# Kernel tuning notes

Measured on AMD Instinct MI355X. Metric: run time of the kernel, lower is better.

## Reference

```python
import jax, jax.numpy as jnp
import numpy as np

B, S, D, C = 16, 1024, 768, 2


def setup_inputs() -> dict:
    key = jax.random.key(0)
    ks = jax.random.split(key, 6)
    sc = 1.0 / np.sqrt(D)
    return {
        "tokens": jax.random.normal(ks[0], (B, S, D), jnp.float32),
        "Wk": jax.random.normal(ks[1], (D, D), jnp.float32) * sc,
        "bk": jnp.zeros((D,), jnp.float32),
        "Wq": jax.random.normal(ks[2], (D, D), jnp.float32) * sc,
        "bq": jnp.zeros((D,), jnp.float32),
        "Wv": jax.random.normal(ks[3], (D, D), jnp.float32) * sc,
        "bv": jnp.zeros((D,), jnp.float32),
        "ln_g": jnp.ones((S, D), jnp.float32),
        "ln_b": jnp.zeros((S, D), jnp.float32),
        "W_sgsa": jax.random.normal(ks[4], (D, 1), jnp.float32) * sc,
        "b_sgsa": jnp.zeros((1,), jnp.float32),
        "W_fnn": jax.random.normal(ks[5], (4 * D, C), jnp.float32) * (1.0 / np.sqrt(4 * D)),
        "b_fnn": jnp.zeros((C,), jnp.float32),
    }


def reference(tokens, Wk, bk, Wq, bq, Wv, bv, ln_g, ln_b, W_sgsa, b_sgsa, W_fnn, b_fnn):
    fact = 1.0 / jnp.sqrt(jnp.asarray(D, tokens.dtype))
    # --- token-wise single-head attention ---
    K = tokens @ Wk + bk                                  # [B,S,D]
    Q = tokens @ Wq + bq
    V = tokens @ Wv + bv
    att = jax.nn.softmax(jnp.einsum('bsd,btd->bst', Q, K) * fact, axis=-1)  # [B,S,S]
    out = jnp.einsum('bst,btd->bsd', att, V)              # [B,S,D]
    # --- LayerNorm over last two dims (S,D) jointly, eps=1e-8 ---
    mu = jnp.mean(out, axis=(1, 2), keepdims=True)
    var = jnp.var(out, axis=(1, 2), keepdims=True)
    out_ln = (out - mu) / jnp.sqrt(var + 1e-8) * ln_g + ln_b
    # --- feature-wise attention (same K/Q/V weights, transposed bmm) ---
    K_N = out_ln @ Wk + bk
    Q_N = out_ln @ Wq + bq
    V_N = out_ln @ Wv + bv
    att_N = jax.nn.softmax(jnp.einsum('bsd,bse->bde', Q_N, K_N) * fact, axis=-1)  # [B,D,D]
    out_N = jnp.einsum('bsd,bde->bse', V_N, att_N)        # [B,S,D]
    # --- SGSA gating ---
    gate = out_N @ W_sgsa + b_sgsa                        # [B,S,1]
    out_sgsa = gate * out_N                               # [B,S,D]
    # --- concat, dual pooling, FC ---
    cat = jnp.concatenate([tokens, out_sgsa], axis=2)     # [B,S,2D]
    pooled = jnp.concatenate([jnp.mean(cat, axis=1), jnp.max(cat, axis=1)], axis=1)  # [B,4D]
    return pooled @ W_fnn + b_fnn                         # [B,C]
```

## Files before the change

### kernel.cpp

```cpp
#include <hip/hip_runtime.h>

#define BB 16
#define SS 1024
#define DD 768

typedef _Float16 f16x4 __attribute__((ext_vector_type(4)));
typedef _Float16 f16x8 __attribute__((ext_vector_type(8)));
typedef float f32x4 __attribute__((ext_vector_type(4)));

__device__ __forceinline__ void gload_lds16(const void* g, void* l) {
  __builtin_amdgcn_global_load_lds(
      (const __attribute__((address_space(1))) unsigned int*)g,
      (__attribute__((address_space(3))) unsigned int*)l, 16, 0, 0);
}

template<int OUTM, int BIAS>
__global__ __launch_bounds__(512) void gemm256(
    const _Float16* __restrict__ A, long long aB,
    const _Float16* __restrict__ Bt, long long bB,
    const float* __restrict__ bias, int biasB,
    void* __restrict__ Cv, long long cB,
    int M, int N, int K)
{
  __shared__ __attribute__((aligned(16))) _Float16 lds[65536];
  const int t = threadIdx.x;
  int z, m0, n0;
  if (OUTM == 3 || OUTM == 4) {
    const int lin = blockIdx.x + 9 * blockIdx.y;
    const int xcd = lin & 7, idx = lin >> 3;
    const int mt  = xcd * 8 + idx / 9;
    const int zn  = idx % 9;
    z  = zn / 3;
    n0 = (zn % 3) * 256;
    m0 = mt * 256;
  } else {
    z = blockIdx.z;
    m0 = blockIdx.x * 256;
    n0 = blockIdx.y * 256;
  }
  const _Float16* Ab = A + (size_t)z * aB;
  const _Float16* Bb = Bt + (size_t)z * bB;

  const int l = t & 63, w = t >> 6;
  const int wr = (w >> 2) * 128, wc = (w & 3) * 64;
  const int lrow = l & 15, kq = l >> 4;
  const int p2 = lrow >> 1;
  const int qread = ((lrow & 1) << 2) | (kq ^ (p2 & 3));
  const int fragoff = p2 * 128 + qread * 16;

  const int sp = t >> 3, sq = t & 7;
  const int srow = 2 * sp + (sq >> 2);
  const int schk = (sq & 3) ^ (sp & 3);
  const size_t ldK = (size_t)K * 2;
  const char* pA0 = (const char*)Ab + (size_t)(m0 + srow) * ldK + schk * 16;
  const char* pA1 = pA0 + (size_t)128 * ldK;
  const char* pB0 = (const char*)Bb + (size_t)(n0 + srow) * ldK + schk * 16;
  const char* pB1 = pB0 + (size_t)128 * ldK;
  char* const ldsb = (char*)lds;
  const int dstt = t * 16;

  auto stg = [&](int mat, int s, int T, int sd) {
    const char* g0 = (mat ? pB0 : pA0) + (size_t)T * 128 + s * 64;
    const char* g1 = (mat ? pB1 : pA1) + (size_t)T * 128 + s * 64;
    char* d = ldsb + sd * 65536 + mat * 32768 + s * 16384 + dstt;
    gload_lds16(g0, d);
    gload_lds16(g1, d + 8192);
  };

  f32x4 acc[8][4] = {};
  f16x8 b0[4], b1[4], a00[4], a01[4], a10[4], a11[4];

  stg(0, 0, 0, 0); stg(1, 0, 0, 0); stg(0, 1, 0, 0); stg(1, 1, 0, 0);

  const int NT = K >> 6;
  for (int T = 0; T < NT; ++T) {
    const int sd = T & 1, sn = sd ^ 1;
    const char* Abase = ldsb + sd * 65536;
    const char* Bbase = Abase + 32768;
    const bool pf = (T + 1) < NT;

    asm volatile("s_waitcnt vmcnt(0)" ::: "memory");
    __builtin_amdgcn_s_barrier();
    asm volatile("" ::: "memory");
    if (pf) {
      stg(0, 0, T + 1, sn); stg(1, 0, T + 1, sn);
      stg(0, 1, T + 1, sn); stg(1, 1, T + 1, sn);
    }

    #pragma unroll
    for (int n = 0; n < 4; n++)
      b0[n]  = *(const f16x8*)(Bbase + (wc + n * 16) * 64 + fragoff);
    #pragma unroll
    for (int mi = 0; mi < 4; mi++)
      a00[mi] = *(const f16x8*)(Abase + (wr + mi * 16) * 64 + fragoff);
    #pragma unroll
    for (int mi = 0; mi < 4; mi++)
      a01[mi] = *(const f16x8*)(Abase + (wr + 64 + mi * 16) * 64 + fragoff);
    #pragma unroll
    for (int n = 0; n < 4; n++)
      b1[n]  = *(const f16x8*)(Bbase + 16384 + (wc + n * 16) * 64 + fragoff);
    #pragma unroll
    for (int mi = 0; mi < 4; mi++)
      a10[mi] = *(const f16x8*)(Abase + 16384 + (wr + mi * 16) * 64 + fragoff);
    #pragma unroll
    for (int mi = 0; mi < 4; mi++)
      a11[mi] = *(const f16x8*)(Abase + 16384 + (wr + 64 + mi * 16) * 64 + fragoff);

    __builtin_amdgcn_s_setprio(1);
    #pragma unroll
    for (int mi = 0; mi < 4; mi++)
      #pragma unroll
      for (int n = 0; n < 4; n++)
        acc[mi][n] = __builtin_amdgcn_mfma_f32_16x16x32_f16(a00[mi], b0[n], acc[mi][n], 0, 0, 0);
    #pragma unroll
    for (int mi = 0; mi < 4; mi++)
      #pragma unroll
      for (int n = 0; n < 4; n++)
        acc[4 + mi][n] = __builtin_amdgcn_mfma_f32_16x16x32_f16(a01[mi], b0[n], acc[4 + mi][n], 0, 0, 0);
    #pragma unroll
    for (int mi = 0; mi < 4; mi++)
      #pragma unroll
      for (int n = 0; n < 4; n++)
        acc[mi][n] = __builtin_amdgcn_mfma_f32_16x16x32_f16(a10[mi], b1[n], acc[mi][n], 0, 0, 0);
    #pragma unroll
    for (int mi = 0; mi < 4; mi++)
      #pragma unroll
      for (int n = 0; n < 4; n++)
        acc[4 + mi][n] = __builtin_amdgcn_mfma_f32_16x16x32_f16(a11[mi], b1[n], acc[4 + mi][n], 0, 0, 0);
    __builtin_amdgcn_s_setprio(0);
  }

  const int crow = (l >> 4) * 4, ccol = l & 15;
  #pragma unroll
  for (int m = 0; m < 8; ++m) {
    const int rq = m0 + wr + (m >> 2) * 64 + (m & 3) * 16 + crow;
    #pragma unroll
    for (int n = 0; n < 4; ++n) {
      const int c = n0 + wc + n * 16 + ccol;
      const float bv = BIAS ? bias[(size_t)z * biasB + c] : 0.0f;
      if (OUTM == 0) {
        float* C = (float*)Cv + (size_t)z * cB;
        #pragma unroll
        for (int j = 0; j < 4; j++)
          C[(size_t)(rq + j) * N + c] = acc[m][n][j] + bv;
      } else {
        _Float16* C = (_Float16*)Cv + (size_t)z * cB;
        const bool tr = (OUTM == 3) ? (z == 2) : (z < 2);
        if (tr) {
          const int bq = rq >> 10, s = rq & 1023;
          f16x4 o;
          #pragma unroll
          for (int j = 0; j < 4; j++) o[j] = (_Float16)(acc[m][n][j] + bv);
          *(f16x4*)&C[((size_t)(bq * N + c) << 10) + s] = o;
        } else {
          #pragma unroll
          for (int j = 0; j < 4; j++)
            C[(size_t)(rq + j) * N + c] = (_Float16)(acc[m][n][j] + bv);
        }
      }
    }
  }
}

__global__ __launch_bounds__(256) void cast_f2h(const float* __restrict__ in,
                                                _Float16* __restrict__ outp, long long n4)
{
  for (long long i = (long long)blockIdx.x * 256 + threadIdx.x; i < n4;
       i += (long long)gridDim.x * 256) {
    float4 v = ((const float4*)in)[i];
    f16x4 r;
    r[0] = (_Float16)v.x; r[1] = (_Float16)v.y; r[2] = (_Float16)v.z; r[3] = (_Float16)v.w;
    ((f16x4*)outp)[i] = r;
  }
}

__global__ __launch_bounds__(256) void transpose_f2h(const float* __restrict__ in,
                                                     _Float16* __restrict__ outp, int R, int C)
{
  __shared__ float tile[32][33];
  const int r0 = blockIdx.y * 32, c0 = blockIdx.x * 32;
  const int tx = threadIdx.x & 31, ty = threadIdx.x >> 5;
  #pragma unroll
  for (int i = 0; i < 4; i++)
    tile[ty + i * 8][tx] = in[(size_t)(r0 + ty + i * 8) * C + c0 + tx];
  __syncthreads();
  #pragma unroll
  for (int i = 0; i < 4; i++)
    outp[(size_t)(c0 + ty + i * 8) * R + r0 + tx] = (_Float16)tile[tx][ty + i * 8];
}

__global__ __launch_bounds__(256) void transpose_b2h(const _Float16* __restrict__ in, long long inB,
                                                     _Float16* __restrict__ outp, long long outB,
                                                     int R, int C)
{
  __shared__ _Float16 tile[32][33];
  const _Float16* ib = in + (size_t)blockIdx.z * inB;
  _Float16* ob = outp + (size_t)blockIdx.z * outB;
  const int r0 = blockIdx.y * 32, c0 = blockIdx.x * 32;
  const int tx = threadIdx.x & 31, ty = threadIdx.x >> 5;
  #pragma unroll
  for (int i = 0; i < 4; i++)
    tile[ty + i * 8][tx] = ib[(size_t)(r0 + ty + i * 8) * C + c0 + tx];
  __syncthreads();
  #pragma unroll
  for (int i = 0; i < 4; i++)
    ob[(size_t)(c0 + ty + i * 8) * R + r0 + tx] = tile[tx][ty + i * 8];
}

__global__ void pack_bias(const float* __restrict__ a, const float* __restrict__ b,
                          const float* __restrict__ c, float* __restrict__ o)
{
  int t = blockIdx.x * 256 + threadIdx.x;
  if (t < 768) o[t] = a[t];
  else if (t < 1536) o[t] = b[t - 768];
  else if (t < 2304) o[t] = c[t - 1536];
}

template<int VPT>
__global__ __launch_bounds__(256) void softmax_f2h(const float* __restrict__ X,
                                                   _Float16* __restrict__ Y,
                                                   int L, float scale)
{
  const size_t base = (size_t)blockIdx.x * L;
  const int t = threadIdx.x;
  float v[VPT];
  float m = -3.4e38f;
  #pragma unroll
  for (int j = 0; j < VPT; j++) { v[j] = X[base + t + j * 256]; m = fmaxf(m, v[j]); }
  __shared__ float red[256];
  red[t] = m; __syncthreads();
  #pragma unroll
  for (int off = 128; off > 0; off >>= 1) {
    if (t < off) red[t] = fmaxf(red[t], red[t + off]);
    __syncthreads();
  }
  m = red[0]; __syncthreads();
  float s = 0.0f;
  #pragma unroll
  for (int j = 0; j < VPT; j++) { v[j] = __expf((v[j] - m) * scale); s += v[j]; }
  red[t] = s; __syncthreads();
  #pragma unroll
  for (int off = 128; off > 0; off >>= 1) {
    if (t < off) red[t] += red[t + off];
    __syncthreads();
  }
  const float inv = 1.0f / red[0];
  #pragma unroll
  for (int j = 0; j < VPT; j++) Y[base + t + j * 256] = (_Float16)(v[j] * inv);
}

__global__ __launch_bounds__(256) void ln_partial(const float* __restrict__ src,
                                                  float* __restrict__ part)
{
  const int b = blockIdx.y, ch = blockIdx.x;
  const float4* p = (const float4*)(src + (size_t)b * SS * DD) + (size_t)ch * 3072;
  const int t = threadIdx.x;
  float s = 0.0f, q = 0.0f;
  #pragma unroll
  for (int i = 0; i < 12; i++) {
    float4 v = p[t + i * 256];
    s += v.x + v.y + v.z + v.w;
    q += v.x * v.x + v.y * v.y + v.z * v.z + v.w * v.w;
  }
  __shared__ float rs[256], rq[256];
  rs[t] = s; rq[t] = q; __syncthreads();
  #pragma unroll
  for (int off = 128; off > 0; off >>= 1) {
    if (t < off) { rs[t] += rs[t + off]; rq[t] += rq[t + off]; }
    __syncthreads();
  }
  if (t == 0) { part[(b * 64 + ch) * 2] = rs[0]; part[(b * 64 + ch) * 2 + 1] = rq[0]; }
}

__global__ void ln_final(const float* __restrict__ part, float* __restrict__ stats)
{
  const int b = blockIdx.x, t = threadIdx.x;
  float s = part[(b * 64 + t) * 2];
  float q = part[(b * 64 + t) * 2 + 1];
  #pragma unroll
  for (int off = 32; off > 0; off >>= 1) { s += __shfl_down(s, off); q += __shfl_down(q, off); }
  if (t == 0) {
    const float invN = 1.0f / (float)(SS * DD);
    float mu = s * invN;
    float var = q * invN - mu * mu;
    stats[b * 2] = mu;
    stats[b * 2 + 1] = rsqrtf(var + 1e-8f);
  }
}

__global__ __launch_bounds__(256) void ln_apply_h(const float* __restrict__ src,
                                                  const float* __restrict__ g,
                                                  const float* __restrict__ bta,
                                                  const float* __restrict__ stats,
                                                  _Float16* __restrict__ dst)
{
  const long long n4 = (long long)BB * SS * DD / 4;
  const int SD4 = SS * DD / 4;
  for (long long i = (long long)blockIdx.x * 256 + threadIdx.x; i < n4;
       i += (long long)gridDim.x * 256) {
    const int b = (int)(i / SD4);
    const int sd4 = (int)(i - (long long)b * SD4);
    const float mu = stats[b * 2], rs = stats[b * 2 + 1];
    float4 v = ((const float4*)src)[i];
    float4 gg = ((const float4*)g)[sd4];
    float4 bb = ((const float4*)bta)[sd4];
    f16x4 r;
    r[0] = (_Float16)((v.x - mu) * rs * gg.x + bb.x);
    r[1] = (_Float16)((v.y - mu) * rs * gg.y + bb.y);
    r[2] = (_Float16)((v.z - mu) * rs * gg.z + bb.z);
    r[3] = (_Float16)((v.w - mu) * rs * gg.w + bb.w);
    ((f16x4*)dst)[i] = r;
  }
}

__global__ __launch_bounds__(256) void gate_k(const float* __restrict__ outN,
                                              const float* __restrict__ wsg,
                                              const float* __restrict__ bsg,
                                              float* __restrict__ gate)
{
  const int row = blockIdx.x * 4 + (threadIdx.x >> 6);
  const int l = threadIdx.x & 63;
  const float* src = outN + (size_t)row * DD;
  float s = 0.0f;
  #pragma unroll
  for (int i = 0; i < 12; i++) s += src[l + i * 64] * wsg[l + i * 64];
  #pragma unroll
  for (int off = 32; off > 0; off >>= 1) s += __shfl_down(s, off);
  if (l == 0) gate[row] = s + bsg[0];
}

__global__ __launch_bounds__(256) void pool_partial(const float* __restrict__ tokens,
                                                    const float* __restrict__ outN,
                                                    const float* __restrict__ gate,
                                                    float* __restrict__ part)
{
  const int b = blockIdx.y, ch = blockIdx.x, t = threadIdx.x;
  float st0 = 0, st1 = 0, st2 = 0, so0 = 0, so1 = 0, so2 = 0;
  float xt0 = -3.4e38f, xt1 = -3.4e38f, xt2 = -3.4e38f;
  float xo0 = -3.4e38f, xo1 = -3.4e38f, xo2 = -3.4e38f;
  const size_t rowbase = ((size_t)b * SS + ch * 32) * DD;
  for (int i = 0; i < 32; i++) {
    const float* tr = tokens + rowbase + (size_t)i * DD;
    const float* orw = outN + rowbase + (size_t)i * DD;
    const float g = gate[b * SS + ch * 32 + i];
    float t0 = tr[t], t1 = tr[t + 256], t2 = tr[t + 512];
    float o0 = orw[t] * g, o1 = orw[t + 256] * g, o2 = orw[t + 512] * g;
    st0 += t0; st1 += t1; st2 += t2;
    so0 += o0; so1 += o1; so2 += o2;
    xt0 = fmaxf(xt0, t0); xt1 = fmaxf(xt1, t1); xt2 = fmaxf(xt2, t2);
    xo0 = fmaxf(xo0, o0); xo1 = fmaxf(xo1, o1); xo2 = fmaxf(xo2, o2);
  }
  float* pb = part + (size_t)(b * 32 + ch) * 3072;
  pb[t] = st0;          pb[t + 256] = st1;          pb[t + 512] = st2;
  pb[768 + t] = so0;    pb[768 + t + 256] = so1;    pb[768 + t + 512] = so2;
  pb[1536 + t] = xt0;   pb[1536 + t + 256] = xt1;   pb[1536 + t + 512] = xt2;
  pb[2304 + t] = xo0;   pb[2304 + t + 256] = xo1;   pb[2304 + t + 512] = xo2;
}

__global__ __launch_bounds__(256) void pool_final(const float* __restrict__ part,
                                                  float* __restrict__ pooled)
{
  const int idx = blockIdx.x * 256 + threadIdx.x;
  const int b = idx / DD, d = idx - b * DD;
  float st = 0, so = 0, xt = -3.4e38f, xo = -3.4e38f;
  for (int ch = 0; ch < 32; ch++) {
    const float* pb = part + (size_t)(b * 32 + ch) * 3072;
    st += pb[d]; so += pb[768 + d];
    xt = fmaxf(xt, pb[1536 + d]); xo = fmaxf(xo, pb[2304 + d]);
  }
  const float inv = 1.0f / (float)SS;
  pooled[(size_t)b * 3072 + d]        = st * inv;
  pooled[(size_t)b * 3072 + 768 + d]  = so * inv;
  pooled[(size_t)b * 3072 + 1536 + d] = xt;
  pooled[(size_t)b * 3072 + 2304 + d] = xo;
}

__global__ __launch_bounds__(256) void fc_k(const float* __restrict__ pooled,
                                            const float* __restrict__ Wf,
                                            const float* __restrict__ bf,
                                            float* __restrict__ outp)
{
  const int b = blockIdx.x, t = threadIdx.x;
  float p0 = 0.0f, p1 = 0.0f;
  #pragma unroll
  for (int i = 0; i < 12; i++) {
    const int j = t + i * 256;
    const float pv = pooled[(size_t)b * 3072 + j];
    p0 += pv * Wf[j * 2];
    p1 += pv * Wf[j * 2 + 1];
  }
  __shared__ float r0[256], r1[256];
  r0[t] = p0; r1[t] = p1; __syncthreads();
  #pragma unroll
  for (int off = 128; off > 0; off >>= 1) {
    if (t < off) { r0[t] += r0[t + off]; r1[t] += r1[t + off]; }
    __syncthreads();
  }
  if (t == 0) {
    outp[b * 2 + 0] = r0[0] + bf[0];
    outp[b * 2 + 1] = r1[0] + bf[1];
  }
}

extern "C" void kernel_launch(void* const* d_in, const int* in_sizes, int n_in,
                              void* d_out, int out_size, void* d_ws, size_t ws_size,
                              hipStream_t stream)
{
  const float* tokens = (const float*)d_in[0];
  const float* Wk  = (const float*)d_in[1];
  const float* bk  = (const float*)d_in[2];
  const float* Wq  = (const float*)d_in[3];
  const float* bq  = (const float*)d_in[4];
  const float* Wv  = (const float*)d_in[5];
  const float* bv  = (const float*)d_in[6];
  const float* lng = (const float*)d_in[7];
  const float* lnb = (const float*)d_in[8];
  const float* Wsg = (const float*)d_in[9];
  const float* bsg = (const float*)d_in[10];
  const float* Wf  = (const float*)d_in[11];
  const float* bfn = (const float*)d_in[12];
  float* outp = (float*)d_out;
  (void)in_sizes; (void)n_in; (void)out_size; (void)ws_size;

  char* ws = (char*)d_ws;
  float*    R0   = (float*)(ws + 0);
  _Float16* R1   = (_Float16*)(ws + 67108864);
  _Float16* R2   = (_Float16*)(ws + 92274688);
  _Float16* R3   = (_Float16*)(ws + 117440512);
  _Float16* R4   = (_Float16*)(ws + 142606336);
  _Float16* R5   = (_Float16*)(ws + 167772160);
  _Float16* Wt   = (_Float16*)(ws + 201326592);
  float* bias3   = (float*)(ws + 204865536);
  float* part    = (float*)(ws + 204874752);
  float* stats   = (float*)(ws + 204882944);
  float* gate    = (float*)(ws + 204883072);
  float* ppart   = (float*)(ws + 204948608);
  float* pooled  = (float*)(ws + 211240064);

  const float fact = 0.036084391824351615f;
  const long long SD = (long long)SS * DD;
  const long long S2 = (long long)SS * SS;
  const long long D2 = (long long)DD * DD;
  const long long PL = (long long)BB * SD;

  cast_f2h<<<2048, 256, 0, stream>>>(tokens, R1, PL / 4);
  transpose_f2h<<<dim3(24, 24), 256, 0, stream>>>(Wk, Wt,               768, 768);
  transpose_f2h<<<dim3(24, 24), 256, 0, stream>>>(Wq, Wt + 589824,      768, 768);
  transpose_f2h<<<dim3(24, 24), 256, 0, stream>>>(Wv, Wt + 2 * 589824,  768, 768);
  pack_bias<<<9, 256, 0, stream>>>(bk, bq, bv, bias3);

  gemm256<3, 1><<<dim3(9, 64, 1), 512, 0, stream>>>(R1, 0, Wt, 589824, bias3, 768,
                                                    (void*)R2, PL, BB * SS, DD, DD);
  gemm256<0, 0><<<dim3(4, 4, 16), 512, 0, stream>>>(R3, SD, R2, SD, nullptr, 0,
                                                    (void*)R0, S2, SS, SS, DD);
  softmax_f2h<4><<<BB * SS, 256, 0, stream>>>(R0, R5, SS, fact);
  gemm256<0, 0><<<dim3(4, 3, 16), 512, 0, stream>>>(R5, S2, R4, SD, nullptr, 0,
                                                    (void*)R0, SD, SS, DD, SS);
  ln_partial<<<dim3(64, 16), 256, 0, stream>>>(R0, part);
  ln_final<<<16, 64, 0, stream>>>(part, stats);
  ln_apply_h<<<2048, 256, 0, stream>>>(R0, lng, lnb, stats, R1);

  gemm256<4, 1><<<dim3(9, 64, 1), 512, 0, stream>>>(R1, 0, Wt, 589824, bias3, 768,
                                                    (void*)R2, PL, BB * SS, DD, DD);
  gemm256<0, 0><<<dim3(3, 3, 16), 512, 0, stream>>>(R3, SD, R2, SD, nullptr, 0,
                                                    (void*)R0, D2, DD, DD, SS);
  softmax_f2h<3><<<BB * DD, 256, 0, stream>>>(R0, R5, DD, fact);
  transpose_b2h<<<dim3(24, 24, 16), 256, 0, stream>>>(R5, D2, R1, D2, DD, DD);
  gemm256<0, 0><<<dim3(4, 3, 16), 512, 0, stream>>>(R4, SD, R1, D2, nullptr, 0,
                                                    (void*)R0, SD, SS, DD, DD);

  gate_k<<<4096, 256, 0, stream>>>(R0, Wsg, bsg, gate);
  pool_partial<<<dim3(32, BB), 256, 0, stream>>>(tokens, R0, gate, ppart);
  pool_final<<<48, 256, 0, stream>>>(ppart, pooled);
  fc_k<<<16, 256, 0, stream>>>(pooled, Wf, bfn, outp);
}
```

Measured before the change: 440.0 us.

## Restructure GEMM main loop into four-phase ping-pong with staggered prefetch

Splits each K-tile iteration of the 256x256 GEMM into four MFMA quadrants, with barriers between them. Each quadrant's global-to-LDS prefetch is issued separately, two tiles ahead for some halves, using partial vmcnt waits instead of a full drain at the top of every iteration. The goal is to overlap LDS fragment reads and global loads with MFMA work and stop stalling on all outstanding loads each step. In exchange it adds many more block barriers per iteration and relies on subtle ordering of when buffers are reused, which risks races or barrier overhead.

```diff
diff --git a/kernel.cpp b/kernel.cpp
--- a/kernel.cpp
+++ b/kernel.cpp
@@ -44,9 +44,9 @@
   const int l = t & 63, w = t >> 6;
   const int wr = (w >> 2) * 128, wc = (w & 3) * 64;
   const int lrow = l & 15, kq = l >> 4;
-  const int p2 = lrow >> 1;
-  const int qread = ((lrow & 1) << 2) | (kq ^ (p2 & 3));
-  const int fragoff = p2 * 128 + qread * 16;
+  const int p2v = lrow >> 1;
+  const int qread = ((lrow & 1) << 2) | (kq ^ (p2v & 3));
+  const int fragoff = p2v * 128 + qread * 16;
 
   const int sp = t >> 3, sq = t & 7;
   const int srow = 2 * sp + (sq >> 2);
@@ -68,67 +68,118 @@
   };
 
   f32x4 acc[8][4] = {};
-  f16x8 b0[4], b1[4], a00[4], a01[4], a10[4], a11[4];
+  f16x8 a00[4], a01[4], a10[4], a11[4];
+  f16x8 b00[2], b01[2], b10[2], b11[2];
+
+#define MF(d, a, b) d = __builtin_amdgcn_mfma_f32_16x16x32_f16(a, b, d, 0, 0, 0)
 
   stg(0, 0, 0, 0); stg(1, 0, 0, 0); stg(0, 1, 0, 0); stg(1, 1, 0, 0);
+  stg(0, 0, 1, 1); stg(1, 0, 1, 1);
+  asm volatile("s_waitcnt vmcnt(4)" ::: "memory");
+  __builtin_amdgcn_s_barrier();
+  asm volatile("" ::: "memory");
 
   const int NT = K >> 6;
   for (int T = 0; T < NT; ++T) {
     const int sd = T & 1, sn = sd ^ 1;
     const char* Abase = ldsb + sd * 65536;
     const char* Bbase = Abase + 32768;
-    const bool pf = (T + 1) < NT;
-
-    asm volatile("s_waitcnt vmcnt(0)" ::: "memory");
+
+    #pragma unroll
+    for (int i = 0; i < 4; i++)
+      a00[i] = *(const f16x8*)(Abase + (wr + i * 16) * 64 + fragoff);
+    #pragma unroll
+    for (int i = 0; i < 4; i++)
+      a01[i] = *(const f16x8*)(Abase + 16384 + (wr + i * 16) * 64 + fragoff);
+    #pragma unroll
+    for (int n = 0; n < 2; n++)
+      b00[n] = *(const f16x8*)(Bbase + (wc + n * 16) * 64 + fragoff);
+    #pragma unroll
+    for (int n = 0; n < 2; n++)
+      b01[n] = *(const f16x8*)(Bbase + 16384 + (wc + n * 16) * 64 + fragoff);
+    if (T + 1 < NT) stg(0, 1, T + 1, sn);
+    __builtin_amdgcn_s_barrier();
+    asm volatile("s_waitcnt lgkmcnt(0)" ::: "memory");
+    __builtin_amdgcn_sched_barrier(0);
+    __builtin_amdgcn_s_setprio(1);
+    #pragma unroll
+    for (int i = 0; i < 4; i++) {
+      MF(acc[i][0], a00[i], b00[0]); MF(acc[i][1], a00[i], b00[1]);
+    }
+    #pragma unroll
+    for (int i = 0; i < 4; i++) {
+      MF(acc[i][0], a01[i], b01[0]); MF(acc[i][1], a01[i], b01[1]);
+    }
+    __builtin_amdgcn_s_setprio(0);
     __builtin_amdgcn_s_barrier();
     asm volatile("" ::: "memory");
-    if (pf) {
-      stg(0, 0, T + 1, sn); stg(1, 0, T + 1, sn);
-      stg(0, 1, T + 1, sn); stg(1, 1, T + 1, sn);
-    }
-
-    #pragma unroll
-    for (int n = 0; n < 4; n++)
-      b0[n]  = *(const f16x8*)(Bbase + (wc + n * 16) * 64 + fragoff);
-    #pragma unroll
-    for (int mi = 0; mi < 4; mi++)
-      a00[mi] = *(const f16x8*)(Abase + (wr + mi * 16) * 64 + fragoff);
-    #pragma unroll
-    for (int mi = 0; mi < 4; mi++)
-      a01[mi] = *(const f16x8*)(Abase + (wr + 64 + mi * 16) * 64 + fragoff);
-    #pragma unroll
-    for (int n = 0; n < 4; n++)
-      b1[n]  = *(const f16x8*)(Bbase + 16384 + (wc + n * 16) * 64 + fragoff);
-    #pragma unroll
-    for (int mi = 0; mi < 4; mi++)
-      a10[mi] = *(const f16x8*)(Abase + 16384 + (wr + mi * 16) * 64 + fragoff);
-    #pragma unroll
-    for (int mi = 0; mi < 4; mi++)
-      a11[mi] = *(const f16x8*)(Abase + 16384 + (wr + 64 + mi * 16) * 64 + fragoff);
-
+
+    #pragma unroll
+    for (int i = 0; i < 4; i++)
+      a10[i] = *(const f16x8*)(Abase + (wr + 64 + i * 16) * 64 + fragoff);
+    #pragma unroll
+    for (int i = 0; i < 4; i++)
+      a11[i] = *(const f16x8*)(Abase + 16384 + (wr + 64 + i * 16) * 64 + fragoff);
+    #pragma unroll
+    for (int n = 0; n < 2; n++)
+      b10[n] = *(const f16x8*)(Bbase + (wc + 32 + n * 16) * 64 + fragoff);
+    #pragma unroll
+    for (int n = 0; n < 2; n++)
+      b11[n] = *(const f16x8*)(Bbase + 16384 + (wc + 32 + n * 16) * 64 + fragoff);
+    if (T + 1 < NT) stg(1, 1, T + 1, sn);
+    __builtin_amdgcn_s_barrier();
+    asm volatile("s_waitcnt lgkmcnt(0)" ::: "memory");
+    __builtin_amdgcn_sched_barrier(0);
     __builtin_amdgcn_s_setprio(1);
     #pragma unroll
-    for (int mi = 0; mi < 4; mi++)
-      #pragma unroll
-      for (int n = 0; n < 4; n++)
-        acc[mi][n] = __builtin_amdgcn_mfma_f32_16x16x32_f16(a00[mi], b0[n], acc[mi][n], 0, 0, 0);
-    #pragma unroll
-    for (int mi = 0; mi < 4; mi++)
-      #pragma unroll
-      for (int n = 0; n < 4; n++)
-        acc[4 + mi][n] = __builtin_amdgcn_mfma_f32_16x16x32_f16(a01[mi], b0[n], acc[4 + mi][n], 0, 0, 0);
-    #pragma unroll
-    for (int mi = 0; mi < 4; mi++)
-      #pragma unroll
-      for (int n = 0; n < 4; n++)
-        acc[mi][n] = __builtin_amdgcn_mfma_f32_16x16x32_f16(a10[mi], b1[n], acc[mi][n], 0, 0, 0);
-    #pragma unroll
-    for (int mi = 0; mi < 4; mi++)
-      #pragma unroll
-      for (int n = 0; n < 4; n++)
-        acc[4 + mi][n] = __builtin_amdgcn_mfma_f32_16x16x32_f16(a11[mi], b1[n], acc[4 + mi][n], 0, 0, 0);
+    for (int i = 0; i < 4; i++) {
+      MF(acc[4 + i][2], a10[i], b10[0]); MF(acc[4 + i][3], a10[i], b10[1]);
+    }
+    #pragma unroll
+    for (int i = 0; i < 4; i++) {
+      MF(acc[4 + i][2], a11[i], b11[0]); MF(acc[4 + i][3], a11[i], b11[1]);
+    }
     __builtin_amdgcn_s_setprio(0);
-  }
+    __builtin_amdgcn_s_barrier();
+    asm volatile("" ::: "memory");
+
+    if (T + 2 < NT) stg(0, 0, T + 2, sd);
+    __builtin_amdgcn_s_barrier();
+    __builtin_amdgcn_sched_barrier(0);
+    __builtin_amdgcn_s_setprio(1);
+    #pragma unroll
+    for (int i = 0; i < 4; i++) {
+      MF(acc[i][2], a00[i], b10[0]); MF(acc[i][3], a00[i], b10[1]);
+    }
+    #pragma unroll
+    for (int i = 0; i < 4; i++) {
+      MF(acc[i][2], a01[i], b11[0]); MF(acc[i][3], a01[i], b11[1]);
+    }
+    __builtin_amdgcn_s_setprio(0);
+    __builtin_amdgcn_s_barrier();
+    asm volatile("" ::: "memory");
+
+    if (T + 2 < NT) stg(1, 0, T + 2, sd);
+    if (T + 1 < NT) {
+      if (T + 1 == NT - 1) asm volatile("s_waitcnt vmcnt(0)" ::: "memory");
+      else                 asm volatile("s_waitcnt vmcnt(4)" ::: "memory");
+    }
+    __builtin_amdgcn_s_barrier();
+    __builtin_amdgcn_sched_barrier(0);
+    __builtin_amdgcn_s_setprio(1);
+    #pragma unroll
+    for (int i = 0; i < 4; i++) {
+      MF(acc[4 + i][0], a10[i], b00[0]); MF(acc[4 + i][1], a10[i], b00[1]);
+    }
+    #pragma unroll
+    for (int i = 0; i < 4; i++) {
+      MF(acc[4 + i][0], a11[i], b01[0]); MF(acc[4 + i][1], a11[i], b01[1]);
+    }
+    __builtin_amdgcn_s_setprio(0);
+    __builtin_amdgcn_s_barrier();
+    asm volatile("" ::: "memory");
+  }
+#undef MF
 
   const int crow = (l >> 4) * 4, ccol = l & 15;
   #pragma unroll
```

Result: slower. 454.0 us (+3.2%).

## Fuse LN stats into GEMM epilogue, fp16 intermediates, move token pooling into cast

Applied to the files above, without the earlier changes.

The attention-output GEMM now writes fp16 and reduces per-block sum and sum-of-squares in its epilogue, which removes the separate ln_partial pass. LayerNorm is applied in place on the fp16 buffer. The final GEMM also writes fp16, so gate and pooling read half the bytes. Token pooling is folded into the fp32-to-fp16 cast kernel, so the fp32 tokens are read once. The cost is fp16 rounding before LayerNorm and pooling, plus an extra block reduction in the GEMM epilogue.

```diff
diff --git a/kernel.cpp b/kernel.cpp
--- a/kernel.cpp
+++ b/kernel.cpp
@@ -20,6 +20,7 @@
     const _Float16* __restrict__ Bt, long long bB,
     const float* __restrict__ bias, int biasB,
     void* __restrict__ Cv, long long cB,
+    float* __restrict__ aux,
     int M, int N, int K)
 {
   __shared__ __attribute__((aligned(16))) _Float16 lds[65536];
@@ -44,9 +45,9 @@
   const int l = t & 63, w = t >> 6;
   const int wr = (w >> 2) * 128, wc = (w & 3) * 64;
   const int lrow = l & 15, kq = l >> 4;
-  const int p2 = lrow >> 1;
-  const int qread = ((lrow & 1) << 2) | (kq ^ (p2 & 3));
-  const int fragoff = p2 * 128 + qread * 16;
+  const int p2v = lrow >> 1;
+  const int qread = ((lrow & 1) << 2) | (kq ^ (p2v & 3));
+  const int fragoff = p2v * 128 + qread * 16;
 
   const int sp = t >> 3, sq = t & 7;
   const int srow = 2 * sp + (sq >> 2);
@@ -143,6 +144,11 @@
         #pragma unroll
         for (int j = 0; j < 4; j++)
           C[(size_t)(rq + j) * N + c] = acc[m][n][j] + bv;
+      } else if (OUTM == 5 || OUTM == 6) {
+        _Float16* C = (_Float16*)Cv + (size_t)z * cB;
+        #pragma unroll
+        for (int j = 0; j < 4; j++)
+          C[(size_t)(rq + j) * N + c] = (_Float16)(acc[m][n][j] + bv);
       } else {
         _Float16* C = (_Float16*)Cv + (size_t)z * cB;
         const bool tr = (OUTM == 3) ? (z == 2) : (z < 2);
@@ -160,18 +166,54 @@
       }
     }
   }
-}
-
-__global__ __launch_bounds__(256) void cast_f2h(const float* __restrict__ in,
-                                                _Float16* __restrict__ outp, long long n4)
-{
-  for (long long i = (long long)blockIdx.x * 256 + threadIdx.x; i < n4;
-       i += (long long)gridDim.x * 256) {
-    float4 v = ((const float4*)in)[i];
-    f16x4 r;
-    r[0] = (_Float16)v.x; r[1] = (_Float16)v.y; r[2] = (_Float16)v.z; r[3] = (_Float16)v.w;
-    ((f16x4*)outp)[i] = r;
-  }
+
+  if (OUTM == 6) {
+    float ls = 0.0f, lq = 0.0f;
+    #pragma unroll
+    for (int m = 0; m < 8; ++m)
+      #pragma unroll
+      for (int n = 0; n < 4; ++n)
+        #pragma unroll
+        for (int j = 0; j < 4; j++) {
+          const float v = acc[m][n][j];
+          ls += v; lq += v * v;
+        }
+    __syncthreads();
+    float* red = (float*)lds;
+    red[t] = ls; red[512 + t] = lq;
+    __syncthreads();
+    #pragma unroll
+    for (int off = 256; off > 0; off >>= 1) {
+      if (t < off) { red[t] += red[t + off]; red[512 + t] += red[512 + t + off]; }
+      __syncthreads();
+    }
+    if (t == 0) {
+      const int chunk = blockIdx.x * 3 + blockIdx.y;
+      aux[(z * 12 + chunk) * 2]     = red[0];
+      aux[(z * 12 + chunk) * 2 + 1] = red[512];
+    }
+  }
+}
+
+__global__ __launch_bounds__(256) void cast_pool(const float* __restrict__ tokens,
+                                                 _Float16* __restrict__ tok_h,
+                                                 float* __restrict__ tpart)
+{
+  const int b = blockIdx.y, ch = blockIdx.x, t = threadIdx.x;
+  float s0 = 0, s1 = 0, s2 = 0;
+  float x0 = -3.4e38f, x1 = -3.4e38f, x2 = -3.4e38f;
+  const size_t rowbase = ((size_t)b * SS + ch * 32) * DD;
+  for (int i = 0; i < 32; i++) {
+    const float* tr = tokens + rowbase + (size_t)i * DD;
+    _Float16* hw = tok_h + rowbase + (size_t)i * DD;
+    float t0 = tr[t], t1 = tr[t + 256], t2 = tr[t + 512];
+    hw[t] = (_Float16)t0; hw[t + 256] = (_Float16)t1; hw[t + 512] = (_Float16)t2;
+    s0 += t0; s1 += t1; s2 += t2;
+    x0 = fmaxf(x0, t0); x1 = fmaxf(x1, t1); x2 = fmaxf(x2, t2);
+  }
+  float* pb = tpart + (size_t)(b * 32 + ch) * 1536;
+  pb[t] = s0;        pb[t + 256] = s1;        pb[t + 512] = s2;
+  pb[768 + t] = x0;  pb[768 + t + 256] = x1;  pb[768 + t + 512] = x2;
 }
 
 __global__ __launch_bounds__(256) void transpose_f2h(const float* __restrict__ in,
@@ -249,34 +291,11 @@
   for (int j = 0; j < VPT; j++) Y[base + t + j * 256] = (_Float16)(v[j] * inv);
 }
 
-__global__ __launch_bounds__(256) void ln_partial(const float* __restrict__ src,
-                                                  float* __restrict__ part)
-{
-  const int b = blockIdx.y, ch = blockIdx.x;
-  const float4* p = (const float4*)(src + (size_t)b * SS * DD) + (size_t)ch * 3072;
-  const int t = threadIdx.x;
+__global__ void ln_final(const float* __restrict__ part, float* __restrict__ stats)
+{
+  const int b = blockIdx.x, t = threadIdx.x;
   float s = 0.0f, q = 0.0f;
-  #pragma unroll
-  for (int i = 0; i < 12; i++) {
-    float4 v = p[t + i * 256];
-    s += v.x + v.y + v.z + v.w;
-    q += v.x * v.x + v.y * v.y + v.z * v.z + v.w * v.w;
-  }
-  __shared__ float rs[256], rq[256];
-  rs[t] = s; rq[t] = q; __syncthreads();
-  #pragma unroll
-  for (int off = 128; off > 0; off >>= 1) {
-    if (t < off) { rs[t] += rs[t + off]; rq[t] += rq[t + off]; }
-    __syncthreads();
-  }
-  if (t == 0) { part[(b * 64 + ch) * 2] = rs[0]; part[(b * 64 + ch) * 2 + 1] = rq[0]; }
-}
-
-__global__ void ln_final(const float* __restrict__ part, float* __restrict__ stats)
-{
-  const int b = blockIdx.x, t = threadIdx.x;
-  float s = part[(b * 64 + t) * 2];
-  float q = part[(b * 64 + t) * 2 + 1];
+  if (t < 12) { s = part[(b * 12 + t) * 2]; q = part[(b * 12 + t) * 2 + 1]; }
   #pragma unroll
   for (int off = 32; off > 0; off >>= 1) { s += __shfl_down(s, off); q += __shfl_down(q, off); }
   if (t == 0) {
@@ -288,11 +307,10 @@
   }
 }
 
-__global__ __launch_bounds__(256) void ln_apply_h(const float* __restrict__ src,
+__global__ __launch_bounds__(256) void ln_apply_h(_Float16* __restrict__ data,
                                                   const float* __restrict__ g,
                                                   const float* __restrict__ bta,
-                                                  const float* __restrict__ stats,
-                                                  _Float16* __restrict__ dst)
+                                                  const float* __restrict__ stats)
 {
   const long long n4 = (long long)BB * SS * DD / 4;
   const int SD4 = SS * DD / 4;
@@ -301,72 +319,66 @@
     const int b = (int)(i / SD4);
     const int sd4 = (int)(i - (long long)b * SD4);
     const float mu = stats[b * 2], rs = stats[b * 2 + 1];
-    float4 v = ((const float4*)src)[i];
+    f16x4 v = ((const f16x4*)data)[i];
     float4 gg = ((const float4*)g)[sd4];
     float4 bb = ((const float4*)bta)[sd4];
     f16x4 r;
-    r[0] = (_Float16)((v.x - mu) * rs * gg.x + bb.x);
-    r[1] = (_Float16)((v.y - mu) * rs * gg.y + bb.y);
-    r[2] = (_Float16)((v.z - mu) * rs * gg.z + bb.z);
-    r[3] = (_Float16)((v.w - mu) * rs * gg.w + bb.w);
-    ((f16x4*)dst)[i] = r;
-  }
-}
-
-__global__ __launch_bounds__(256) void gate_k(const float* __restrict__ outN,
+    r[0] = (_Float16)(((float)v[0] - mu) * rs * gg.x + bb.x);
+    r[1] = (_Float16)(((float)v[1] - mu) * rs * gg.y + bb.y);
+    r[2] = (_Float16)(((float)v[2] - mu) * rs * gg.z + bb.z);
+    r[3] = (_Float16)(((float)v[3] - mu) * rs * gg.w + bb.w);
+    ((f16x4*)data)[i] = r;
+  }
+}
+
+__global__ __launch_bounds__(256) void gate_k(const _Float16* __restrict__ outN,
                                               const float* __restrict__ wsg,
                                               const float* __restrict__ bsg,
                                               float* __restrict__ gate)
 {
   const int row = blockIdx.x * 4 + (threadIdx.x >> 6);
   const int l = threadIdx.x & 63;
-  const float* src = outN + (size_t)row * DD;
+  const _Float16* src = outN + (size_t)row * DD;
   float s = 0.0f;
   #pragma unroll
-  for (int i = 0; i < 12; i++) s += src[l + i * 64] * wsg[l + i * 64];
+  for (int i = 0; i < 12; i++) s += (float)src[l + i * 64] * wsg[l + i * 64];
   #pragma unroll
   for (int off = 32; off > 0; off >>= 1) s += __shfl_down(s, off);
   if (l == 0) gate[row] = s + bsg[0];
 }
 
-__global__ __launch_bounds__(256) void pool_partial(const float* __restrict__ tokens,
-                                                    const float* __restrict__ outN,
-                                                    const float* __restrict__ gate,
-                                                    float* __restrict__ part)
+__global__ __launch_bounds__(256) void opool(const _Float16* __restrict__ outN,
+                                             const float* __restrict__ gate,
+                                             float* __restrict__ opart)
 {
   const int b = blockIdx.y, ch = blockIdx.x, t = threadIdx.x;
-  float st0 = 0, st1 = 0, st2 = 0, so0 = 0, so1 = 0, so2 = 0;
-  float xt0 = -3.4e38f, xt1 = -3.4e38f, xt2 = -3.4e38f;
-  float xo0 = -3.4e38f, xo1 = -3.4e38f, xo2 = -3.4e38f;
+  float s0 = 0, s1 = 0, s2 = 0;
+  float x0 = -3.4e38f, x1 = -3.4e38f, x2 = -3.4e38f;
   const size_t rowbase = ((size_t)b * SS + ch * 32) * DD;
   for (int i = 0; i < 32; i++) {
-    const float* tr = tokens + rowbase + (size_t)i * DD;
-    const float* orw = outN + rowbase + (size_t)i * DD;
+    const _Float16* orw = outN + rowbase + (size_t)i * DD;
     const float g = gate[b * SS + ch * 32 + i];
-    float t0 = tr[t], t1 = tr[t + 256], t2 = tr[t + 512];
-    float o0 = orw[t] * g, o1 = orw[t + 256] * g, o2 = orw[t + 512] * g;
-    st0 += t0; st1 += t1; st2 += t2;
-    so0 += o0; so1 += o1; so2 += o2;
-    xt0 = fmaxf(xt0, t0); xt1 = fmaxf(xt1, t1); xt2 = fmaxf(xt2, t2);
-    xo0 = fmaxf(xo0, o0); xo1 = fmaxf(xo1, o1); xo2 = fmaxf(xo2, o2);
-  }
-  float* pb = part + (size_t)(b * 32 + ch) * 3072;
-  pb[t] = st0;          pb[t + 256] = st1;          pb[t + 512] = st2;
-  pb[768 + t] = so0;    pb[768 + t + 256] = so1;    pb[768 + t + 512] = so2;
-  pb[1536 + t] = xt0;   pb[1536 + t + 256] = xt1;   pb[1536 + t + 512] = xt2;
-  pb[2304 + t] = xo0;   pb[2304 + t + 256] = xo1;   pb[2304 + t + 512] = xo2;
-}
-
-__global__ __launch_bounds__(256) void pool_final(const float* __restrict__ part,
+    float o0 = (float)orw[t] * g, o1 = (float)orw[t + 256] * g, o2 = (float)orw[t + 512] * g;
+    s0 += o0; s1 += o1; s2 += o2;
+    x0 = fmaxf(x0, o0); x1 = fmaxf(x1, o1); x2 = fmaxf(x2, o2);
+  }
+  float* pb = opart + (size_t)(b * 32 + ch) * 1536;
+  pb[t] = s0;        pb[t + 256] = s1;        pb[t + 512] = s2;
+  pb[768 + t] = x0;  pb[768 + t + 256] = x1;  pb[768 + t + 512] = x2;
+}
+
+__global__ __launch_bounds__(256) void pool_final(const float* __restrict__ tpart,
+                                                  const float* __restrict__ opart,
                                                   float* __restrict__ pooled)
 {
   const int idx = blockIdx.x * 256 + threadIdx.x;
   const int b = idx / DD, d = idx - b * DD;
   float st = 0, so = 0, xt = -3.4e38f, xo = -3.4e38f;
   for (int ch = 0; ch < 32; ch++) {
-    const float* pb = part + (size_t)(b * 32 + ch) * 3072;
-    st += pb[d]; so += pb[768 + d];
-    xt = fmaxf(xt, pb[1536 + d]); xo = fmaxf(xo, pb[2304 + d]);
+    const float* tb = tpart + (size_t)(b * 32 + ch) * 1536;
+    const float* ob = opart + (size_t)(b * 32 + ch) * 1536;
+    st += tb[d]; xt = fmaxf(xt, tb[768 + d]);
+    so += ob[d]; xo = fmaxf(xo, ob[768 + d]);
   }
   const float inv = 1.0f / (float)SS;
   pooled[(size_t)b * 3072 + d]        = st * inv;
@@ -431,11 +443,12 @@
   _Float16* R5   = (_Float16*)(ws + 167772160);
   _Float16* Wt   = (_Float16*)(ws + 201326592);
   float* bias3   = (float*)(ws + 204865536);
-  float* part    = (float*)(ws + 204874752);
-  float* stats   = (float*)(ws + 204882944);
-  float* gate    = (float*)(ws + 204883072);
-  float* ppart   = (float*)(ws + 204948608);
-  float* pooled  = (float*)(ws + 211240064);
+  float* lnpart  = (float*)(ws + 204874752);
+  float* stats   = (float*)(ws + 204878848);
+  float* gate    = (float*)(ws + 204878976);
+  float* tpart   = (float*)(ws + 204944512);
+  float* opart   = (float*)(ws + 208090240);
+  float* pooled  = (float*)(ws + 211235968);
 
   const float fact = 0.036084391824351615f;
   const long long SD = (long long)SS * DD;
@@ -443,34 +456,33 @@
   const long long D2 = (long long)DD * DD;
   const long long PL = (long long)BB * SD;
 
-  cast_f2h<<<2048, 256, 0, stream>>>(tokens, R1, PL / 4);
+  cast_pool<<<dim3(32, BB), 256, 0, stream>>>(tokens, R1, tpart);
   transpose_f2h<<<dim3(24, 24), 256, 0, stream>>>(Wk, Wt,               768, 768);
   transpose_f2h<<<dim3(24, 24), 256, 0, stream>>>(Wq, Wt + 589824,      768, 768);
   transpose_f2h<<<dim3(24, 24), 256, 0, stream>>>(Wv, Wt + 2 * 589824,  768, 768);
   pack_bias<<<9, 256, 0, stream>>>(bk, bq, bv, bias3);
 
   gemm256<3, 1><<<dim3(9, 64, 1), 512, 0, stream>>>(R1, 0, Wt, 589824, bias3, 768,
-                                                    (void*)R2, PL, BB * SS, DD, DD);
+                                                    (void*)R2, PL, nullptr, BB * SS, DD, DD);
   gemm256<0, 0><<<dim3(4, 4, 16), 512, 0, stream>>>(R3, SD, R2, SD, nullptr, 0,
-                                                    (void*)R0, S2, SS, SS, DD);
+                                                    (void*)R0, S2, nullptr, SS, SS, DD);
   softmax_f2h<4><<<BB * SS, 256, 0, stream>>>(R0, R5, SS, fact);
-  gemm256<0, 0><<<dim3(4, 3, 16), 512, 0, stream>>>(R5, S2, R4, SD, nullptr, 0,
-                                                    (void*)R0, SD, SS, DD, SS);
-  ln_partial<<<dim3(64, 16), 256, 0, stream>>>(R0, part);
-  ln_final<<<16, 64, 0, stream>>>(part, stats);
-  ln_apply_h<<<2048, 256, 0, stream>>>(R0, lng, lnb, stats, R1);
+  gemm256<6, 0><<<dim3(4, 3, 16), 512, 0, stream>>>(R5, S2, R4, SD, nullptr, 0,
+                                                    (void*)R1, SD, lnpart, SS, DD, SS);
+  ln_final<<<16, 64, 0, stream>>>(lnpart, stats);
+  ln_apply_h<<<2048, 256, 0, stream>>>(R1, lng, lnb, stats);
 
   gemm256<4, 1><<<dim3(9, 64, 1), 512, 0, stream>>>(R1, 0, Wt, 589824, bias3, 768,
-                                                    (void*)R2, PL, BB * SS, DD, DD);
+                                                    (void*)R2, PL, nullptr, BB * SS, DD, DD);
   gemm256<0, 0><<<dim3(3, 3, 16), 512, 0, stream>>>(R3, SD, R2, SD, nullptr, 0,
-                                                    (void*)R0, D2, DD, DD, SS);
+                                                    (void*)R0, D2, nullptr, DD, DD, SS);
   softmax_f2h<3><<<BB * DD, 256, 0, stream>>>(R0, R5, DD, fact);
   transpose_b2h<<<dim3(24, 24, 16), 256, 0, stream>>>(R5, D2, R1, D2, DD, DD);
-  gemm256<0, 0><<<dim3(4, 3, 16), 512, 0, stream>>>(R4, SD, R1, D2, nullptr, 0,
-                                                    (void*)R0, SD, SS, DD, DD);
-
-  gate_k<<<4096, 256, 0, stream>>>(R0, Wsg, bsg, gate);
-  pool_partial<<<dim3(32, BB), 256, 0, stream>>>(tokens, R0, gate, ppart);
-  pool_final<<<48, 256, 0, stream>>>(ppart, pooled);
+  gemm256<5, 0><<<dim3(4, 3, 16), 512, 0, stream>>>(R4, SD, R1, D2, nullptr, 0,
+                                                    (void*)R5, SD, nullptr, SS, DD, DD);
+
+  gate_k<<<4096, 256, 0, stream>>>(R5, Wsg, bsg, gate);
+  opool<<<dim3(32, BB), 256, 0, stream>>>(R5, gate, opart);
+  pool_final<<<48, 256, 0, stream>>>(tpart, opart, pooled);
   fc_k<<<16, 256, 0, stream>>>(pooled, Wf, bfn, outp);
 }
```

New measurement: 418.0 us. 5.0% less time.
